# Optimization experiments

Measured on AMD Instinct MI355X. Metric: run time of the kernel, lower is better.

## Reference

```python
import jax, jax.numpy as jnp
import numpy as np

N, F, FE = 50000, 128, 1
E, EI, G = 800000, 400000, 64
NEG_SLOPE = 0.01


def _linear_params(key, out_dim, in_dim):
    k1, k2 = jax.random.split(key)
    bound = 1.0 / np.sqrt(in_dim)
    w = jax.random.uniform(k1, (out_dim, in_dim), jnp.float32, -bound, bound)
    b = jax.random.uniform(k2, (out_dim,), jnp.float32, -bound, bound)
    return w, b


def setup_inputs() -> dict:
    key = jax.random.key(0)
    ks = jax.random.split(key, 16)
    inp = {
        'x': jax.random.normal(ks[0], (N, F), jnp.float32),
        'edge_index': jax.random.randint(ks[1], (2, E), 0, N, jnp.int64) if jax.config.read('jax_enable_x64') else jax.random.randint(ks[1], (2, E), 0, N, jnp.int32),
        'edge_attr': jax.random.normal(ks[2], (E, FE), jnp.float32),
        'internal_edge_index': jax.random.randint(ks[3], (2, EI), 0, N, jnp.int32),
        'internal_edge_attr': jax.random.normal(ks[4], (EI, FE), jnp.float32),
        'batch': jnp.sort(jax.random.randint(ks[5], (N,), 0, G, jnp.int32)),
    }
    # four conv sub-modules: message Linear(2F+FE -> 1), update Linear(F+1 -> F)
    names = ['e1', 'e2', 'i1', 'i2']
    for i, nm in enumerate(names):
        wm, bm = _linear_params(ks[6 + i], 1, 2 * F + FE)
        wu, bu = _linear_params(ks[10 + i], F, F + 1)
        inp[f'wm_{nm}'], inp[f'bm_{nm}'] = wm, bm
        inp[f'wu_{nm}'], inp[f'bu_{nm}'] = wu, bu
    inp['fc1_w'], inp['fc1_b'] = _linear_params(ks[14], 128, 2 * F)
    inp['fc2_w'], inp['fc2_b'] = _linear_params(ks[15], 1, 128)
    return inp


def _conv(x, edge_index, edge_attr, wm, bm, wu, bu):
    s, d = edge_index[0], edge_index[1]
    # gather + tiny linear: [E, 2F+FE] @ [2F+FE, 1]
    msg_in = jnp.concatenate([x[s], x[d], edge_attr], axis=1)
    msg = msg_in @ wm.T + bm                      # [E, 1]
    msg = jax.nn.leaky_relu(msg, NEG_SLOPE)
    msg = jax.nn.softmax(msg, axis=1)             # [E,1] -> all ones (faithful)
    node_msg = jax.ops.segment_sum(msg, s, num_segments=x.shape[0])  # [N, 1]
    upd = jnp.concatenate([x, node_msg], axis=1) @ wu.T + bu          # [N, F]
    upd = jax.nn.leaky_relu(upd, NEG_SLOPE)
    return jax.nn.softmax(upd, axis=1)


def _scatter_mean(x, seg, num_segments):
    s = jax.ops.segment_sum(x, seg, num_segments=num_segments)
    c = jax.ops.segment_sum(jnp.ones((x.shape[0], 1), x.dtype), seg, num_segments=num_segments)
    return s / jnp.maximum(c, 1.0)


def reference(x, edge_index, edge_attr, internal_edge_index, internal_edge_attr, batch,
              wm_e1, bm_e1, wu_e1, bu_e1, wm_e2, bm_e2, wu_e2, bu_e2,
              wm_i1, bm_i1, wu_i1, bu_i1, wm_i2, bm_i2, wu_i2, bu_i2,
              fc1_w, fc1_b, fc2_w, fc2_b):
    ext = _conv(x, edge_index, edge_attr, wm_e1, bm_e1, wu_e1, bu_e1)
    ext = _conv(ext, edge_index, edge_attr, wm_e2, bm_e2, wu_e2, bu_e2)
    itn = _conv(x, internal_edge_index, internal_edge_attr, wm_i1, bm_i1, wu_i1, bu_i1)
    itn = _conv(itn, internal_edge_index, internal_edge_attr, wm_i2, bm_i2, wu_i2, bu_i2)
    ez = _scatter_mean(ext, batch, G)             # [G, F]
    iz = _scatter_mean(itn, batch, G)             # [G, F]
    z = jnp.concatenate([ez, iz], axis=1)         # [G, 2F]
    z = jax.nn.relu(z @ fc1_w.T + fc1_b)
    return z @ fc2_w.T + fc2_b                    # [G, 1]
```

## Files before the change

### kernel.cpp

```cpp
#include <hip/hip_runtime.h>
#include <hip/hip_bf16.h>

#define NN  50000
#define FD  128
#define NE  800000
#define NEI 400000
#define NG  64

#define EZ_STRIDE  8192
#define CNT_STRIDE 64
#define DEGB_WORDS 12544

#define HB_E 32
#define HB_I 16
#define HB_SLICE 6250

typedef short  short8 __attribute__((ext_vector_type(8)));
typedef float  f32x4  __attribute__((ext_vector_type(4)));

union S8 { short8 s; unsigned int u[4]; };

__device__ __forceinline__ unsigned short bf16h(float f) {
  unsigned int u = __float_as_uint(f);
  u += 0x7FFFu + ((u >> 16) & 1u);
  return (unsigned short)(u >> 16);
}
__device__ __forceinline__ float bf16tof(unsigned short h) {
  return __uint_as_float(((unsigned int)h) << 16);
}
__device__ __forceinline__ unsigned int pk_bf16(float a, float b) {
  __hip_bfloat162 h = __float22bfloat162_rn(make_float2(a, b));
  unsigned int u;
  __builtin_memcpy(&u, &h, 4);
  return u;
}
__device__ __forceinline__ float frcp(float x) { return __builtin_amdgcn_rcpf(x); }

#define AB_BAT 13
#define AB_PRE 8

__global__ __launch_bounds__(256) void aux_kernel(
    const int4* __restrict__ ei4, const int4* __restrict__ iei4,
    const int* __restrict__ batch,
    const float* __restrict__ wu_e1, const float* __restrict__ wu_e2,
    const float* __restrict__ wu_i1, const float* __restrict__ wu_i2,
    unsigned int* __restrict__ degp,
    int* __restrict__ cnt,
    unsigned short* __restrict__ WB, float* __restrict__ wcolp, int ncopy)
{
  __shared__ __align__(16) unsigned char SM[DEGB_WORDS * 4];
  __shared__ int hb[64];
  unsigned int* H  = (unsigned int*)SM;
  float*        WS = (float*)SM;
  const int b = blockIdx.x, t = threadIdx.x;

  if (b < HB_E + HB_I) {
    for (int i = t; i < DEGB_WORDS; i += 256) H[i] = 0;
    __syncthreads();
    if (b < HB_E) {
      const int beg = b * HB_SLICE;
      const int end = min(beg + HB_SLICE, NE / 4);
      for (int i = beg + t; i < end; i += 256) {
        const int4 v = ei4[i];
        atomicAdd(&H[v.x >> 2], 1u << (8 * (v.x & 3)));
        atomicAdd(&H[v.y >> 2], 1u << (8 * (v.y & 3)));
        atomicAdd(&H[v.z >> 2], 1u << (8 * (v.z & 3)));
        atomicAdd(&H[v.w >> 2], 1u << (8 * (v.w & 3)));
      }
    } else {
      const int beg = (b - HB_E) * HB_SLICE;
      const int end = min(beg + HB_SLICE, NEI / 4);
      for (int i = beg + t; i < end; i += 256) {
        const int4 v = iei4[i];
        atomicAdd(&H[v.x >> 2], 1u << (8 * (v.x & 3)));
        atomicAdd(&H[v.y >> 2], 1u << (8 * (v.y & 3)));
        atomicAdd(&H[v.z >> 2], 1u << (8 * (v.z & 3)));
        atomicAdd(&H[v.w >> 2], 1u << (8 * (v.w & 3)));
      }
    }
    __syncthreads();
    unsigned int* dst = degp + (size_t)b * DEGB_WORDS;
    for (int i = t; i < DEGB_WORDS; i += 256) dst[i] = H[i];
  } else if (b < HB_E + HB_I + AB_BAT) {
    const int cp = b & (ncopy - 1);
    if (t < 64) hb[t] = 0;
    __syncthreads();
    const int base = (b - HB_E - HB_I) * 4096 + t;
    for (int u = 0; u < 16; ++u) {
      const int i = base + u * 256;
      if (i < NN) atomicAdd(&hb[batch[i]], 1);
    }
    __syncthreads();
    if (t < 64 && hb[t]) atomicAdd(&cnt[cp * CNT_STRIDE + t], hb[t]);
  } else {
    const int pb = b - HB_E - HB_I - AB_BAT;
    const int c  = pb >> 1;
    const int h  = pb & 1;
    const float* wu = (c == 0) ? wu_e1 : (c == 1) ? wu_e2 : (c == 2) ? wu_i1 : wu_i2;
    for (int idx = t; idx < 64 * 129; idx += 256)
      WS[idx] = wu[(size_t)h * 64 * 129 + idx];
    __syncthreads();
    const int lane = t & 63, u = t >> 6;
    const int n = lane & 15, quad = lane >> 4;
    const int ct = 4 * h + u;
    unsigned short* wb = WB + c * 32768;
    #pragma unroll
    for (int kc = 0; kc < 4; ++kc) {
      const int k0 = kc * 32 + quad * 8;
      const float* src = &WS[(u * 16 + n) * 129 + k0];
      short8 hi, lo;
      #pragma unroll
      for (int e = 0; e < 8; ++e) {
        const float v = src[e];
        const unsigned short hh = bf16h(v);
        hi[e] = (short)hh;
        lo[e] = (short)bf16h(v - bf16tof(hh));
      }
      const int fbase = ((ct * 4 + kc) * 2) * 512 + lane * 8;
      *(short8*)&wb[fbase]       = hi;
      *(short8*)&wb[fbase + 512] = lo;
    }
    if (t < 64) wcolp[c * 128 + h * 64 + t] = WS[t * 129 + 128];
  }
}

__global__ __launch_bounds__(256) void merge_deg_kernel(
    const unsigned int* __restrict__ degp, unsigned int* __restrict__ degb)
{
  const int w = blockIdx.x * 256 + threadIdx.x;
  if (w < DEGB_WORDS) {
    unsigned s = 0;
    #pragma unroll 4
    for (int c = 0; c < HB_E; ++c) s += degp[(size_t)c * DEGB_WORDS + w];
    degb[w] = s;
  } else if (w < 2 * DEGB_WORDS) {
    const int ww = w - DEGB_WORDS;
    unsigned s = 0;
    #pragma unroll 4
    for (int c = 0; c < HB_I; ++c) s += degp[(size_t)(HB_E + c) * DEGB_WORDS + ww];
    degb[w] = s;
  }
}

#define ROWS 32

__global__ __launch_bounds__(256, 4) void conv_mfma_kernel(
    const float* __restrict__ x,
    const unsigned int* __restrict__ degb_ext,
    const unsigned int* __restrict__ degb_int,
    const int* __restrict__ batch,
    const unsigned short* __restrict__ WB, const float* __restrict__ wcolp,
    const float* __restrict__ bu_e1, const float* __restrict__ bu_e2,
    const float* __restrict__ bu_i1, const float* __restrict__ bu_i2,
    float* __restrict__ ez_sum, float* __restrict__ iz_sum, int ncopy)
{
  __shared__ unsigned short XT[2][4096];
  __shared__ float degsE[ROWS];
  __shared__ float degsI[ROWS];
  __shared__ int   bg[ROWS];
  __shared__ float redA[ROWS * 4];
  __shared__ float redB[ROWS * 4];

  const int tid  = threadIdx.x;
  const int lane = tid & 63;
  const int w    = tid >> 6;
  const int n    = lane & 15;
  const int q    = lane >> 4;
  const int mbase = blockIdx.x * ROWS;
  const int cp = blockIdx.x & (ncopy - 1);
  const int jA = w * 16 + n;
  const int jB = (w + 4) * 16 + n;

#define LOADP(C, KC, P) do {                                                  \
    const unsigned short* _p = WB + (C) * 32768 + (w * 4 + (KC)) * 1024 + lane * 8; \
    P[0] = *(const short8*)&_p[0];     P[1] = *(const short8*)&_p[512];       \
    P[2] = *(const short8*)&_p[16384]; P[3] = *(const short8*)&_p[16896];     \
  } while (0)

#define PSTEP(XB, KC, P, ACC) do {                                            \
    _Pragma("unroll")                                                          \
    for (int rt = 0; rt < 2; ++rt) {                                           \
      const short8 Ah = *(const short8*)&XT[XB][((rt * 4 + (KC)) * 64 + lane) * 8]; \
      f32x4 c0 = ACC[rt][0];                                                   \
      c0 = __builtin_amdgcn_mfma_f32_16x16x32_bf16(Ah, P[0], c0, 0, 0, 0);     \
      c0 = __builtin_amdgcn_mfma_f32_16x16x32_bf16(Ah, P[1], c0, 0, 0, 0);     \
      ACC[rt][0] = c0;                                                         \
      f32x4 c1 = ACC[rt][1];                                                   \
      c1 = __builtin_amdgcn_mfma_f32_16x16x32_bf16(Ah, P[2], c1, 0, 0, 0);     \
      c1 = __builtin_amdgcn_mfma_f32_16x16x32_bf16(Ah, P[3], c1, 0, 0, 0);     \
      ACC[rt][1] = c1;                                                         \
    }                                                                          \
  } while (0)

#define PASS(XB, C, ACC) do {                                                 \
    PSTEP(XB, 0, Pa, ACC);                                                    \
    LOADP(C, 2, Pa);                                                          \
    PSTEP(XB, 1, Pb, ACC);                                                    \
    LOADP(C, 3, Pb);                                                          \
    PSTEP(XB, 2, Pa, ACC);                                                    \
    PSTEP(XB, 3, Pb, ACC);                                                    \
  } while (0)

  short8 Pa[4], Pb[4];
  LOADP(0, 0, Pa);
  LOADP(0, 1, Pb);
  const float wcE1A = wcolp[0 * 128 + jA], wcE1B = wcolp[0 * 128 + jB];
  const float wcE2A = wcolp[1 * 128 + jA], wcE2B = wcolp[1 * 128 + jB];
  const float wcI1A = wcolp[2 * 128 + jA], wcI1B = wcolp[2 * 128 + jB];
  const float wcI2A = wcolp[3 * 128 + jA], wcI2B = wcolp[3 * 128 + jB];
  const float bE1A = bu_e1[jA], bE1B = bu_e1[jB];
  const float bE2A = bu_e2[jA], bE2B = bu_e2[jB];
  const float bI1A = bu_i1[jA], bI1B = bu_i1[jB];
  const float bI2A = bu_i2[jA], bI2B = bu_i2[jB];

  #pragma unroll
  for (int u = 0; u < 2; ++u) {
    const int oct  = u * 256 + tid;
    const int frag = oct >> 6, l = oct & 63;
    const int row  = (frag >> 2) * 16 + (l & 15);
    const int k0   = (frag & 3) * 32 + (l >> 4) * 8;
    const int node = mbase + row;
    float4 a = make_float4(0.f, 0.f, 0.f, 0.f), bb = a;
    if (node < NN) {
      const float* xr = x + (size_t)node * FD + k0;
      a  = *(const float4*)xr;
      bb = *(const float4*)(xr + 4);
    }
    S8 hi;
    hi.u[0] = pk_bf16(a.x, a.y);
    hi.u[1] = pk_bf16(a.z, a.w);
    hi.u[2] = pk_bf16(bb.x, bb.y);
    hi.u[3] = pk_bf16(bb.z, bb.w);
    *(short8*)&XT[0][oct * 8] = hi.s;
  }
  if (tid < ROWS) {
    const int node = mbase + tid;
    const bool v = node < NN;
    const int nc = v ? node : (NN - 1);
    const unsigned de = (degb_ext[nc >> 2] >> (8 * (nc & 3))) & 255u;
    const unsigned di = (degb_int[nc >> 2] >> (8 * (nc & 3))) & 255u;
    degsE[tid] = v ? (float)de : 0.f;
    degsI[tid] = v ? (float)di : 0.f;
    bg[tid]    = batch[nc];
  }
  __syncthreads();

  f32x4 aE[2][2], aI[2][2];
  #pragma unroll
  for (int rt = 0; rt < 2; ++rt)
    #pragma unroll
    for (int s = 0; s < 2; ++s) {
      aE[rt][s] = (f32x4){0.f, 0.f, 0.f, 0.f};
      aI[rt][s] = (f32x4){0.f, 0.f, 0.f, 0.f};
    }
  PASS(0, 0, aE);
  LOADP(2, 0, Pa);
  LOADP(2, 1, Pb);
  PASS(0, 2, aI);

  #pragma unroll
  for (int rt = 0; rt < 2; ++rt) {
    const float4 dE = *(const float4*)&degsE[rt * 16 + 4 * q];
    const float4 dI = *(const float4*)&degsI[rt * 16 + 4 * q];
    const float dEv[4] = {dE.x, dE.y, dE.z, dE.w};
    const float dIv[4] = {dI.x, dI.y, dI.z, dI.w};
    #pragma unroll
    for (int r = 0; r < 4; ++r) {
      float v;
      v = aE[rt][0][r] + bE1A + dEv[r] * wcE1A; v = fmaxf(v, 0.01f * v); aE[rt][0][r] = __expf(v);
      v = aE[rt][1][r] + bE1B + dEv[r] * wcE1B; v = fmaxf(v, 0.01f * v); aE[rt][1][r] = __expf(v);
      v = aI[rt][0][r] + bI1A + dIv[r] * wcI1A; v = fmaxf(v, 0.01f * v); aI[rt][0][r] = __expf(v);
      v = aI[rt][1][r] + bI1B + dIv[r] * wcI1B; v = fmaxf(v, 0.01f * v); aI[rt][1][r] = __expf(v);
    }
  }

  #pragma unroll
  for (int rt = 0; rt < 2; ++rt) {
    #pragma unroll
    for (int r = 0; r < 4; ++r) {
      float te = aE[rt][0][r] + aE[rt][1][r];
      float ti = aI[rt][0][r] + aI[rt][1][r];
      te += __shfl_xor(te, 1); ti += __shfl_xor(ti, 1);
      te += __shfl_xor(te, 2); ti += __shfl_xor(ti, 2);
      te += __shfl_xor(te, 4); ti += __shfl_xor(ti, 4);
      te += __shfl_xor(te, 8); ti += __shfl_xor(ti, 8);
      if (n == 0) {
        redA[(rt * 16 + q * 4 + r) * 4 + w] = te;
        redB[(rt * 16 + q * 4 + r) * 4 + w] = ti;
      }
    }
  }

  unsigned int pE[2][2][2], pI[2][2][2];
  #pragma unroll
  for (int rt = 0; rt < 2; ++rt)
    #pragma unroll
    for (int s = 0; s < 2; ++s) {
      pE[rt][s][0] = pk_bf16(aE[rt][s][0], aE[rt][s][1]);
      pE[rt][s][1] = pk_bf16(aE[rt][s][2], aE[rt][s][3]);
      pI[rt][s][0] = pk_bf16(aI[rt][s][0], aI[rt][s][1]);
      pI[rt][s][1] = pk_bf16(aI[rt][s][2], aI[rt][s][3]);
    }
  LOADP(1, 0, Pa);
  LOADP(1, 1, Pb);

  #pragma unroll
  for (int rt = 0; rt < 2; ++rt)
    #pragma unroll
    for (int s = 0; s < 2; ++s) {
      const int ct = w + s * 4;
      const int ib = ((rt * 4 + (ct >> 1)) * 64 + ((ct & 1) * 2 + (n >> 3)) * 16 + q * 4) * 8 + (n & 7);
      XT[1][ib]      = (unsigned short)(pE[rt][s][0] & 0xFFFFu);
      XT[1][ib + 8]  = (unsigned short)(pE[rt][s][0] >> 16);
      XT[1][ib + 16] = (unsigned short)(pE[rt][s][1] & 0xFFFFu);
      XT[1][ib + 24] = (unsigned short)(pE[rt][s][1] >> 16);
    }
  __syncthreads();

  #pragma unroll
  for (int rt = 0; rt < 2; ++rt)
    #pragma unroll
    for (int s = 0; s < 2; ++s) {
      const int ct = w + s * 4;
      const int ib = ((rt * 4 + (ct >> 1)) * 64 + ((ct & 1) * 2 + (n >> 3)) * 16 + q * 4) * 8 + (n & 7);
      XT[0][ib]      = (unsigned short)(pI[rt][s][0] & 0xFFFFu);
      XT[0][ib + 8]  = (unsigned short)(pI[rt][s][0] >> 16);
      XT[0][ib + 16] = (unsigned short)(pI[rt][s][1] & 0xFFFFu);
      XT[0][ib + 24] = (unsigned short)(pI[rt][s][1] >> 16);
    }

  float s1iE, s1iI;
  {
    const int rl = (lane & 31) * 4;
    const f32x4 a0 = *(const f32x4*)&redA[rl];
    s1iE = frcp((a0[0] + a0[1]) + (a0[2] + a0[3]));
    const f32x4 b0 = *(const f32x4*)&redB[rl];
    s1iI = frcp((b0[0] + b0[1]) + (b0[2] + b0[3]));
  }

  f32x4 cE[2][2], cI[2][2];
  #pragma unroll
  for (int rt = 0; rt < 2; ++rt)
    #pragma unroll
    for (int s = 0; s < 2; ++s) cE[rt][s] = (f32x4){0.f, 0.f, 0.f, 0.f};
  PASS(1, 1, cE);
  LOADP(3, 0, Pa);
  LOADP(3, 1, Pb);
  __syncthreads();

  #pragma unroll
  for (int rt = 0; rt < 2; ++rt)
    #pragma unroll
    for (int s = 0; s < 2; ++s) cI[rt][s] = (f32x4){0.f, 0.f, 0.f, 0.f};
  PASS(0, 3, cI);

  #pragma unroll
  for (int rt = 0; rt < 2; ++rt) {
    const float4 dE = *(const float4*)&degsE[rt * 16 + 4 * q];
    const float4 dI = *(const float4*)&degsI[rt * 16 + 4 * q];
    const float dEv[4] = {dE.x, dE.y, dE.z, dE.w};
    const float dIv[4] = {dI.x, dI.y, dI.z, dI.w};
    #pragma unroll
    for (int r = 0; r < 4; ++r) {
      const int row = rt * 16 + q * 4 + r;
      const float i1e = __shfl(s1iE, row);
      const float i1i = __shfl(s1iI, row);
      float v;
      v = cE[rt][0][r] * i1e + bE2A + dEv[r] * wcE2A; v = fmaxf(v, 0.01f * v); cE[rt][0][r] = __expf(v);
      v = cE[rt][1][r] * i1e + bE2B + dEv[r] * wcE2B; v = fmaxf(v, 0.01f * v); cE[rt][1][r] = __expf(v);
      v = cI[rt][0][r] * i1i + bI2A + dIv[r] * wcI2A; v = fmaxf(v, 0.01f * v); cI[rt][0][r] = __expf(v);
      v = cI[rt][1][r] * i1i + bI2B + dIv[r] * wcI2B; v = fmaxf(v, 0.01f * v); cI[rt][1][r] = __expf(v);
    }
    #pragma unroll
    for (int r = 0; r < 4; ++r) {
      float te = cE[rt][0][r] + cE[rt][1][r];
      float ti = cI[rt][0][r] + cI[rt][1][r];
      te += __shfl_xor(te, 1); ti += __shfl_xor(ti, 1);
      te += __shfl_xor(te, 2); ti += __shfl_xor(ti, 2);
      te += __shfl_xor(te, 4); ti += __shfl_xor(ti, 4);
      te += __shfl_xor(te, 8); ti += __shfl_xor(ti, 8);
      if (n == 0) {
        redA[(rt * 16 + q * 4 + r) * 4 + w] = te;
        redB[(rt * 16 + q * 4 + r) * 4 + w] = ti;
      }
    }
  }
  __syncthreads();

  float s2iE, s2iI;
  {
    const int rl = (lane & 31) * 4;
    const f32x4 a0 = *(const f32x4*)&redA[rl];
    s2iE = frcp((a0[0] + a0[1]) + (a0[2] + a0[3]));
    const f32x4 b0 = *(const f32x4*)&redB[rl];
    s2iI = frcp((b0[0] + b0[1]) + (b0[2] + b0[3]));
  }
  #pragma unroll
  for (int rt = 0; rt < 2; ++rt) {
    #pragma unroll
    for (int r = 0; r < 4; ++r) {
      const int row = rt * 16 + q * 4 + r;
      const float i2e = __shfl(s2iE, row);
      const float i2i = __shfl(s2iI, row);
      cE[rt][0][r] *= i2e; cE[rt][1][r] *= i2e;
      cI[rt][0][r] *= i2i; cI[rt][1][r] *= i2i;
    }
  }

  {
    float* __restrict__ ezp = ez_sum + (size_t)cp * EZ_STRIDE;
    float* __restrict__ izp = iz_sum + (size_t)cp * EZ_STRIDE;

    if (mbase + ROWS - 1 >= NN) {
      #pragma unroll
      for (int rt = 0; rt < 2; ++rt)
        #pragma unroll
        for (int r = 0; r < 4; ++r) {
          const int row = rt * 16 + q * 4 + r;
          if (mbase + row >= NN) {
            cE[rt][0][r] = 0.f; cE[rt][1][r] = 0.f;
            cI[rt][0][r] = 0.f; cI[rt][1][r] = 0.f;
          }
        }
    }

    const int g0 = bg[0], g1 = bg[ROWS - 1];
    for (int g = g0; g <= g1; ++g) {
      const bool one = (g0 == g1);
      float seA = 0.f, siA = 0.f, seB = 0.f, siB = 0.f;
      #pragma unroll
      for (int rt = 0; rt < 2; ++rt)
        #pragma unroll
        for (int r = 0; r < 4; ++r) {
          const int row = rt * 16 + q * 4 + r;
          const bool m = one || (bg[row] == g);
          seA += m ? cE[rt][0][r] : 0.f;
          seB += m ? cE[rt][1][r] : 0.f;
          siA += m ? cI[rt][0][r] : 0.f;
          siB += m ? cI[rt][1][r] : 0.f;
        }
      seA += __shfl_xor(seA, 16); siA += __shfl_xor(siA, 16);
      seB += __shfl_xor(seB, 16); siB += __shfl_xor(siB, 16);
      seA += __shfl_xor(seA, 32); siA += __shfl_xor(siA, 32);
      seB += __shfl_xor(seB, 32); siB += __shfl_xor(siB, 32);
      if (q == 0) {
        atomicAdd(&ezp[g * FD + jA], seA);
        atomicAdd(&ezp[g * FD + jB], seB);
        atomicAdd(&izp[g * FD + jA], siA);
        atomicAdd(&izp[g * FD + jB], siB);
      }
    }
  }
#undef LOADP
#undef PSTEP
#undef PASS
}

__global__ __launch_bounds__(128) void fc_kernel(
    const float* __restrict__ ez_sum, const float* __restrict__ iz_sum,
    const int* __restrict__ cnt,
    const float* __restrict__ fc1_w, const float* __restrict__ fc1_b,
    const float* __restrict__ fc2_w, const float* __restrict__ fc2_b,
    float* __restrict__ out, int ncopy)
{
  __shared__ float z[256];
  __shared__ float red2[2];
  const int g = blockIdx.x, t = threadIdx.x;
  int cc = 0;
  float se = 0.f, si = 0.f;
  for (int c = 0; c < ncopy; ++c) {
    cc += cnt[c * CNT_STRIDE + g];
    se += ez_sum[(size_t)c * EZ_STRIDE + g * 128 + t];
    si += iz_sum[(size_t)c * EZ_STRIDE + g * 128 + t];
  }
  const float denom = fmaxf((float)cc, 1.0f);
  z[t]       = se / denom;
  z[128 + t] = si / denom;
  __syncthreads();

  const float* wr = fc1_w + (size_t)t * 256;
  float a = fc1_b[t];
  #pragma unroll 4
  for (int c = 0; c < 256; c += 4) {
    const float4 wv = *(const float4*)(wr + c);
    a += wv.x * z[c] + wv.y * z[c + 1] + wv.z * z[c + 2] + wv.w * z[c + 3];
  }
  a = fmaxf(a, 0.f) * fc2_w[t];
  a += __shfl_xor(a, 1);
  a += __shfl_xor(a, 2);
  a += __shfl_xor(a, 4);
  a += __shfl_xor(a, 8);
  a += __shfl_xor(a, 16);
  a += __shfl_xor(a, 32);
  if ((t & 63) == 0) red2[t >> 6] = a;
  __syncthreads();
  if (t == 0) out[g] = red2[0] + red2[1] + fc2_b[0];
}

extern "C" void kernel_launch(void* const* d_in, const int* in_sizes, int n_in,
                              void* d_out, int out_size, void* d_ws, size_t ws_size,
                              hipStream_t stream) {
  const float* x     = (const float*)d_in[0];
  const int4*  ei4   = (const int4*) d_in[1];
  const int4*  iei4  = (const int4*) d_in[3];
  const int*   batch = (const int*)  d_in[5];
  const float* wu_e1 = (const float*)d_in[8];
  const float* bu_e1 = (const float*)d_in[9];
  const float* wu_e2 = (const float*)d_in[12];
  const float* bu_e2 = (const float*)d_in[13];
  const float* wu_i1 = (const float*)d_in[16];
  const float* bu_i1 = (const float*)d_in[17];
  const float* wu_i2 = (const float*)d_in[20];
  const float* bu_i2 = (const float*)d_in[21];
  const float* fc1_w = (const float*)d_in[22];
  const float* fc1_b = (const float*)d_in[23];
  const float* fc2_w = (const float*)d_in[24];
  const float* fc2_b = (const float*)d_in[25];

  const size_t need8 = 8ull * (2 * 32768 + 256) + 2 * (DEGB_WORDS * 4)
                     + 262144 + 2048 + (size_t)(HB_E + HB_I) * DEGB_WORDS * 4;
  const int ncopy = (ws_size >= need8) ? 8 : 1;

  char* ws = (char*)d_ws;
  size_t off = 0;
  float* ez      = (float*)(ws + off); off += (size_t)ncopy * 32768;
  float* iz      = (float*)(ws + off); off += (size_t)ncopy * 32768;
  int*   cnt     = (int*)(ws + off);  off += (size_t)ncopy * 256;
  const size_t zero_bytes = off;
  unsigned int* degb = (unsigned int*)(ws + off); off += 2 * DEGB_WORDS * 4;
  unsigned short* WB = (unsigned short*)(ws + off); off += 262144;
  float* wcolp   = (float*)(ws + off); off += 2048;
  unsigned int* degp = (unsigned int*)(ws + off);
  off += (size_t)(HB_E + HB_I) * DEGB_WORDS * 4;

  hipMemsetAsync(d_ws, 0, zero_bytes, stream);

  aux_kernel<<<HB_E + HB_I + AB_BAT + AB_PRE, 256, 0, stream>>>(
      ei4, iei4, batch, wu_e1, wu_e2, wu_i1, wu_i2,
      degp, cnt, WB, wcolp, ncopy);

  merge_deg_kernel<<<(2 * DEGB_WORDS + 255) / 256, 256, 0, stream>>>(
      degp, degb);

  conv_mfma_kernel<<<dim3((NN + ROWS - 1) / ROWS), 256, 0, stream>>>(
      x, degb, degb + DEGB_WORDS, batch, WB, wcolp,
      bu_e1, bu_e2, bu_i1, bu_i2, ez, iz, ncopy);

  fc_kernel<<<NG, 128, 0, stream>>>(ez, iz, cnt, fc1_w, fc1_b, fc2_w, fc2_b,
                                    (float*)d_out, ncopy);
}
```

Before: 180.0 us.

## Drop memset and degree-merge kernel; fold zeroing and merging into other kernels

```diff
diff --git a/kernel.cpp b/kernel.cpp
--- a/kernel.cpp
+++ b/kernel.cpp
@@ -8,12 +8,16 @@
 #define NG  64
 
 #define EZ_STRIDE  8192
-#define CNT_STRIDE 64
+#define CNT_SLOTS  13
 #define DEGB_WORDS 12544
 
 #define HB_E 32
 #define HB_I 16
 #define HB_SLICE 6250
+
+#define AB_BAT 13
+#define AB_PRE 8
+#define AB_ZERO 8
 
 typedef short  short8 __attribute__((ext_vector_type(8)));
 typedef float  f32x4  __attribute__((ext_vector_type(4)));
@@ -35,9 +39,6 @@
   return u;
 }
 __device__ __forceinline__ float frcp(float x) { return __builtin_amdgcn_rcpf(x); }
-
-#define AB_BAT 13
-#define AB_PRE 8
 
 __global__ __launch_bounds__(256) void aux_kernel(
     const int4* __restrict__ ei4, const int4* __restrict__ iei4,
@@ -46,7 +47,8 @@
     const float* __restrict__ wu_i1, const float* __restrict__ wu_i2,
     unsigned int* __restrict__ degp,
     int* __restrict__ cnt,
-    unsigned short* __restrict__ WB, float* __restrict__ wcolp, int ncopy)
+    unsigned short* __restrict__ WB, float* __restrict__ wcolp,
+    int4* __restrict__ zbuf, int zquads)
 {
   __shared__ __align__(16) unsigned char SM[DEGB_WORDS * 4];
   __shared__ int hb[64];
@@ -82,17 +84,17 @@
     unsigned int* dst = degp + (size_t)b * DEGB_WORDS;
     for (int i = t; i < DEGB_WORDS; i += 256) dst[i] = H[i];
   } else if (b < HB_E + HB_I + AB_BAT) {
-    const int cp = b & (ncopy - 1);
+    const int ib = b - HB_E - HB_I;
     if (t < 64) hb[t] = 0;
     __syncthreads();
-    const int base = (b - HB_E - HB_I) * 4096 + t;
+    const int base = ib * 4096 + t;
     for (int u = 0; u < 16; ++u) {
       const int i = base + u * 256;
       if (i < NN) atomicAdd(&hb[batch[i]], 1);
     }
     __syncthreads();
-    if (t < 64 && hb[t]) atomicAdd(&cnt[cp * CNT_STRIDE + t], hb[t]);
-  } else {
+    if (t < 64) cnt[ib * 64 + t] = hb[t];
+  } else if (b < HB_E + HB_I + AB_BAT + AB_PRE) {
     const int pb = b - HB_E - HB_I - AB_BAT;
     const int c  = pb >> 1;
     const int h  = pb & 1;
@@ -121,24 +123,10 @@
       *(short8*)&wb[fbase + 512] = lo;
     }
     if (t < 64) wcolp[c * 128 + h * 64 + t] = WS[t * 129 + 128];
-  }
-}
-
-__global__ __launch_bounds__(256) void merge_deg_kernel(
-    const unsigned int* __restrict__ degp, unsigned int* __restrict__ degb)
-{
-  const int w = blockIdx.x * 256 + threadIdx.x;
-  if (w < DEGB_WORDS) {
-    unsigned s = 0;
-    #pragma unroll 4
-    for (int c = 0; c < HB_E; ++c) s += degp[(size_t)c * DEGB_WORDS + w];
-    degb[w] = s;
-  } else if (w < 2 * DEGB_WORDS) {
-    const int ww = w - DEGB_WORDS;
-    unsigned s = 0;
-    #pragma unroll 4
-    for (int c = 0; c < HB_I; ++c) s += degp[(size_t)(HB_E + c) * DEGB_WORDS + ww];
-    degb[w] = s;
+  } else {
+    const int zb = b - HB_E - HB_I - AB_BAT - AB_PRE;
+    for (int i = zb * 256 + t; i < zquads; i += AB_ZERO * 256)
+      zbuf[i] = make_int4(0, 0, 0, 0);
   }
 }
 
@@ -146,8 +134,7 @@
 
 __global__ __launch_bounds__(256, 4) void conv_mfma_kernel(
     const float* __restrict__ x,
-    const unsigned int* __restrict__ degb_ext,
-    const unsigned int* __restrict__ degb_int,
+    const unsigned int* __restrict__ degp,
     const int* __restrict__ batch,
     const unsigned short* __restrict__ WB, const float* __restrict__ wcolp,
     const float* __restrict__ bu_e1, const float* __restrict__ bu_e2,
@@ -233,15 +220,27 @@
     hi.u[3] = pk_bf16(bb.z, bb.w);
     *(short8*)&XT[0][oct * 8] = hi.s;
   }
-  if (tid < ROWS) {
-    const int node = mbase + tid;
-    const bool v = node < NN;
-    const int nc = v ? node : (NN - 1);
-    const unsigned de = (degb_ext[nc >> 2] >> (8 * (nc & 3))) & 255u;
-    const unsigned di = (degb_int[nc >> 2] >> (8 * (nc & 3))) & 255u;
-    degsE[tid] = v ? (float)de : 0.f;
-    degsI[tid] = v ? (float)di : 0.f;
-    bg[tid]    = batch[nc];
+  {
+    const int node = tid >> 3, c = tid & 7;
+    const int gn = mbase + node;
+    const bool v = gn < NN;
+    const int nc = v ? gn : (NN - 1);
+    const int wrd = nc >> 2, sh = 8 * (nc & 3);
+    unsigned pe = 0, pi = 0;
+    #pragma unroll
+    for (int k = 0; k < 4; ++k)
+      pe += (degp[(size_t)(c + 8 * k) * DEGB_WORDS + wrd] >> sh) & 255u;
+    #pragma unroll
+    for (int k = 0; k < 2; ++k)
+      pi += (degp[(size_t)(HB_E + c + 8 * k) * DEGB_WORDS + wrd] >> sh) & 255u;
+    float fe = (float)pe, fi = (float)pi;
+    #pragma unroll
+    for (int s = 1; s < 8; s <<= 1) { fe += __shfl_xor(fe, s); fi += __shfl_xor(fi, s); }
+    if (c == 0) {
+      degsE[node] = v ? fe : 0.f;
+      degsI[node] = v ? fi : 0.f;
+      bg[node]    = batch[nc];
+    }
   }
   __syncthreads();
 
@@ -467,9 +466,10 @@
   __shared__ float red2[2];
   const int g = blockIdx.x, t = threadIdx.x;
   int cc = 0;
+  #pragma unroll
+  for (int c = 0; c < CNT_SLOTS; ++c) cc += cnt[c * 64 + g];
   float se = 0.f, si = 0.f;
   for (int c = 0; c < ncopy; ++c) {
-    cc += cnt[c * CNT_STRIDE + g];
     se += ez_sum[(size_t)c * EZ_STRIDE + g * 128 + t];
     si += iz_sum[(size_t)c * EZ_STRIDE + g * 128 + t];
   }
@@ -517,33 +517,27 @@
   const float* fc2_w = (const float*)d_in[24];
   const float* fc2_b = (const float*)d_in[25];
 
-  const size_t need8 = 8ull * (2 * 32768 + 256) + 2 * (DEGB_WORDS * 4)
-                     + 262144 + 2048 + (size_t)(HB_E + HB_I) * DEGB_WORDS * 4;
+  const size_t need8 = 8ull * 2 * 32768 + CNT_SLOTS * 256 + 262144 + 2048
+                     + (size_t)(HB_E + HB_I) * DEGB_WORDS * 4;
   const int ncopy = (ws_size >= need8) ? 8 : 1;
 
   char* ws = (char*)d_ws;
   size_t off = 0;
   float* ez      = (float*)(ws + off); off += (size_t)ncopy * 32768;
   float* iz      = (float*)(ws + off); off += (size_t)ncopy * 32768;
-  int*   cnt     = (int*)(ws + off);  off += (size_t)ncopy * 256;
-  const size_t zero_bytes = off;
-  unsigned int* degb = (unsigned int*)(ws + off); off += 2 * DEGB_WORDS * 4;
+  const int zquads = (int)(((size_t)ncopy * 2 * 32768) / 16);
+  int*   cnt     = (int*)(ws + off);  off += CNT_SLOTS * 256;
   unsigned short* WB = (unsigned short*)(ws + off); off += 262144;
   float* wcolp   = (float*)(ws + off); off += 2048;
   unsigned int* degp = (unsigned int*)(ws + off);
   off += (size_t)(HB_E + HB_I) * DEGB_WORDS * 4;
 
-  hipMemsetAsync(d_ws, 0, zero_bytes, stream);
-
-  aux_kernel<<<HB_E + HB_I + AB_BAT + AB_PRE, 256, 0, stream>>>(
+  aux_kernel<<<HB_E + HB_I + AB_BAT + AB_PRE + AB_ZERO, 256, 0, stream>>>(
       ei4, iei4, batch, wu_e1, wu_e2, wu_i1, wu_i2,
-      degp, cnt, WB, wcolp, ncopy);
-
-  merge_deg_kernel<<<(2 * DEGB_WORDS + 255) / 256, 256, 0, stream>>>(
-      degp, degb);
+      degp, cnt, WB, wcolp, (int4*)ez, zquads);
 
   conv_mfma_kernel<<<dim3((NN + ROWS - 1) / ROWS), 256, 0, stream>>>(
-      x, degb, degb + DEGB_WORDS, batch, WB, wcolp,
+      x, degp, batch, WB, wcolp,
       bu_e1, bu_e2, bu_i1, bu_i2, ez, iz, ncopy);
 
   fc_kernel<<<NG, 128, 0, stream>>>(ez, iz, cnt, fc1_w, fc1_b, fc2_w, fc2_b,
```

After: 170.2 us. 1.06x faster.
